# Kernel optimization log

Hardware: AMD Instinct MI355X
Metric: run time of the kernel (lower is better)

The kernel has to match this reference:

```python
import jax, jax.numpy as jnp
import numpy as np

B, CIN, COUT, K, H, W = 4, 16, 16, 3, 128, 128


def setup_inputs() -> dict:
    key = jax.random.key(0)
    k1, k2, k3 = jax.random.split(key, 3)
    x = jax.random.normal(k1, (B, CIN, H, W), dtype=jnp.float32)
    # kaiming_uniform_(a=1.0): bound = sqrt(6 / ((1 + a^2) * fan_in)), fan_in = Cin*k*k
    fan_in = CIN * K * K
    bound = float(np.sqrt(6.0 / (2.0 * fan_in)))
    weights = jax.random.uniform(k2, (H, W, COUT, CIN, K, K), dtype=jnp.float32,
                                 minval=-bound, maxval=bound)
    bias = jax.random.normal(k3, (H, W, COUT), dtype=jnp.float32)
    return {"x": x, "weights": weights, "bias": bias}


def _xonv2d(x, weights, bias):
    b, c, h, w = x.shape
    k = weights.shape[-1]
    pad = k // 2
    if k % 2 == 1:
        xp = jnp.pad(x, ((0, 0), (0, 0), (pad, pad), (pad, pad)))
    else:
        xp = jnp.pad(x, ((0, 0), (0, 0), (pad - 1, pad), (pad - 1, pad)))
    # Unfold: patch element order matches torch view -> (c, kh, kw) flattened.
    # Stack k*k shifted views: (B, C, k*k, H, W)
    shifts = [xp[:, :, i:i + h, j:j + w] for i in range(k) for j in range(k)]
    patches = jnp.stack(shifts, axis=2)
    wflat = weights.reshape(h, w, weights.shape[2], c, k * k)  # (H,W,O,C,p)
    # out[b,o,h,w] = sum_{c,p} patches[b,c,p,h,w] * wflat[h,w,o,c,p]
    out = jnp.einsum('bcphw,hwocp->bohw', patches, wflat)
    out = out + jnp.transpose(bias, (2, 0, 1))[None]  # (1,O,H,W)
    return out


def reference(x, weights, bias):
    return _xonv2d(x, weights, bias)
```

## Files before the change

### kernel.cpp

```cpp
#include <hip/hip_runtime.h>


#define HWD   128
#define CIND  16
#define COUTD 16
#define SPW   8
#define WPB   4
#define XROWF 44

typedef float f4  __attribute__((ext_vector_type(4)));
typedef float f4u __attribute__((ext_vector_type(4), aligned(4)));

__device__ __forceinline__ void gload_lds16(const f4* gsrc, f4* ldst) {
    __builtin_amdgcn_global_load_lds(
        (const __attribute__((address_space(1))) unsigned int*)gsrc,
        (__attribute__((address_space(3))) unsigned int*)ldst,
        16, 0, 0);
}

__global__ __launch_bounds__(256) void xonv2d_kernel(
    const float* __restrict__ x,
    const float* __restrict__ wts,
    const float* __restrict__ bias,
    float* __restrict__ out)
{
    __shared__ float xs[192 * XROWF];
    __shared__ f4 wbuf[WPB][576];

    const int tid  = threadIdx.x;
    const int lane = tid & 63;
    const int wv   = tid >> 6;

    const int xcd  = blockIdx.x & 7;
    const int idx  = blockIdx.x >> 3;
    const int sblk = xcd * 2048 + idx * 32;
    const int h    = sblk >> 7;
    const int w0b  = sblk & 127;
    const int w0   = w0b + wv * 8;

    const int o  = lane & 15;
    const int g  = lane >> 4;
    const int c0 = g * 4;

    #pragma unroll
    for (int j = 0; j < 8; ++j) {
        const int t = tid + 256 * j;
        if (t < 1920) {
            const int R = t / 10, q = t - R * 10;
            const int b = R / 48;
            const int u = R - b * 48;
            const int c = u / 3, r = u - c * 3;
            const int hy = h + r - 1;
            const int cb = w0b - 4 + 4 * q;
            f4 v = {0.f, 0.f, 0.f, 0.f};
            if (((unsigned)hy < (unsigned)HWD) & ((unsigned)cb <= (unsigned)(HWD - 4)))
                v = *(const f4u*)(x + ((size_t)(b * CIND + c) * HWD + hy) * HWD + cb);
            *(f4*)&xs[R * XROWF + q * 4] = v;
        }
    }

    float bvr[SPW];
    #pragma unroll
    for (int s = 0; s < SPW; ++s)
        bvr[s] = bias[(size_t)(sblk + wv * 8 + s) * COUTD + o];

    const f4* gw0 = (const f4*)wts + (size_t)(sblk + wv * 8) * 576;
    #pragma unroll
    for (int j = 0; j < 9; ++j)
        gload_lds16(gw0 + j * 64 + lane, &wbuf[wv][j * 64]);

    __syncthreads();

    f4 rsA, rsB;

    #pragma unroll
    for (int s = 0; s < SPW; ++s) {
        if (s > 0) asm volatile("s_waitcnt vmcnt(0)" ::: "memory");
        __builtin_amdgcn_sched_barrier(0);

        f4 wvr[9];
        {
            const f4* lp = &wbuf[wv][o * 36 + g * 9];
            #pragma unroll
            for (int j = 0; j < 9; ++j) wvr[j] = lp[j];
        }
        asm volatile("s_waitcnt lgkmcnt(0)" ::: "memory");
        __builtin_amdgcn_sched_barrier(0);

        if (s + 1 < SPW) {
            const f4* gw = gw0 + (size_t)(s + 1) * 576;
            #pragma unroll
            for (int j = 0; j < 9; ++j)
                gload_lds16(gw + j * 64 + lane, &wbuf[wv][j * 64]);
        }
        __builtin_amdgcn_sched_barrier(0);

        const float* wf = (const float*)wvr;
        const int slot0 = wv * 8 + s + 3;
        float acc[4] = {0.f, 0.f, 0.f, 0.f};
        #pragma unroll
        for (int cc = 0; cc < 4; ++cc) {
            #pragma unroll
            for (int b = 0; b < 4; ++b) {
                #pragma unroll
                for (int r = 0; r < 3; ++r) {
                    const int R = (b * CIND + c0 + cc) * 3 + r;
                    const float* xp = &xs[R * XROWF + slot0];
                    const float* wr = wf + cc * 9 + r * 3;
                    acc[b] = fmaf(xp[0], wr[0], acc[b]);
                    acc[b] = fmaf(xp[1], wr[1], acc[b]);
                    acc[b] = fmaf(xp[2], wr[2], acc[b]);
                }
            }
        }

        float rr[4];
        #pragma unroll
        for (int b = 0; b < 4; ++b) {
            float v = acc[b];
            v += __shfl_xor(v, 32);
            v += __shfl_xor(v, 16);
            rr[b] = v;
        }
        const float vout = (g == 0) ? rr[0] : (g == 1) ? rr[1]
                         : (g == 2) ? rr[2] : rr[3];
        const float ov = vout + bvr[s];
        if (s < 4) rsA[s] = ov; else rsB[s - 4] = ov;
    }

    float* ob = out + ((size_t)(g * COUTD + o)) * (HWD * HWD) + h * HWD + w0;
    *(f4*)(ob)     = rsA;
    *(f4*)(ob + 4) = rsB;
}

extern "C" void kernel_launch(void* const* d_in, const int* in_sizes, int n_in,
                              void* d_out, int out_size, void* d_ws, size_t ws_size,
                              hipStream_t stream) {
    const float* x    = (const float*)d_in[0];
    const float* wts  = (const float*)d_in[1];
    const float* bias = (const float*)d_in[2];
    float* out = (float*)d_out;

    const int blocks = (HWD * HWD) / (WPB * SPW);
    xonv2d_kernel<<<blocks, WPB * 64, 0, stream>>>(x, wts, bias, out);
}
```

Baseline: 229.0 us.

## Load weights directly into registers with double-buffered prefetch, drop LDS staging

Removes the LDS weight buffer and the global_load_lds path. Each lane now loads its own 9 contiguous f4 weights straight into registers, with two register buffers so the loads for site s+2 are in flight while site s computes. The lane mapping is swapped (o = lane>>2, g = lane&3), which makes each lane's weight slice contiguous and turns the cross-group reduction into xor-1/2 shuffles. This trades LDS traffic and lgkm waits for higher register pressure and per-lane 16-byte global loads.

```diff
diff --git a/kernel.cpp b/kernel.cpp
--- a/kernel.cpp
+++ b/kernel.cpp
@@ -11,12 +11,52 @@
 typedef float f4  __attribute__((ext_vector_type(4)));
 typedef float f4u __attribute__((ext_vector_type(4), aligned(4)));
 
-__device__ __forceinline__ void gload_lds16(const f4* gsrc, f4* ldst) {
-    __builtin_amdgcn_global_load_lds(
-        (const __attribute__((address_space(1))) unsigned int*)gsrc,
-        (__attribute__((address_space(3))) unsigned int*)ldst,
-        16, 0, 0);
-}
+#define SITE_ITER(S, CUR)                                                     \
+  {                                                                           \
+       \
+       \
+    if ((S) == SPW - 1) asm volatile("s_waitcnt vmcnt(0)" ::: "memory");      \
+    else                asm volatile("s_waitcnt vmcnt(9)" ::: "memory");      \
+    __builtin_amdgcn_sched_barrier(0);                                        \
+    const float* wf = (const float*)(CUR);                                    \
+    const int slot0 = wv * 8 + (S) + 3;                                       \
+    float acc0 = 0.f, acc1 = 0.f, acc2 = 0.f, acc3 = 0.f;                     \
+    _Pragma("unroll")                                                         \
+    for (int cc = 0; cc < 4; ++cc) {                                          \
+      _Pragma("unroll")                                                       \
+      for (int r = 0; r < 3; ++r) {                                           \
+        const float* wr = wf + cc * 9 + r * 3;                                \
+        _Pragma("unroll")                                                     \
+        for (int b = 0; b < 4; ++b) {                                         \
+          const int R = (b * CIND + c0 + cc) * 3 + r;                         \
+          const float* xp = &xs[R * XROWF + slot0];                           \
+          float* ac = (b == 0) ? &acc0 : (b == 1) ? &acc1                     \
+                    : (b == 2) ? &acc2 : &acc3;                               \
+          *ac = fmaf(xp[0], wr[0], *ac);                                      \
+          *ac = fmaf(xp[1], wr[1], *ac);                                      \
+          *ac = fmaf(xp[2], wr[2], *ac);                                      \
+        }                                                                     \
+      }                                                                       \
+    }                                                                         \
+                \
+    acc0 += __shfl_xor(acc0, 1); acc0 += __shfl_xor(acc0, 2);                 \
+    acc1 += __shfl_xor(acc1, 1); acc1 += __shfl_xor(acc1, 2);                 \
+    acc2 += __shfl_xor(acc2, 1); acc2 += __shfl_xor(acc2, 2);                 \
+    acc3 += __shfl_xor(acc3, 1); acc3 += __shfl_xor(acc3, 2);                 \
+    const float vout = (g == 0) ? acc0 : (g == 1) ? acc1                      \
+                     : (g == 2) ? acc2 : acc3;                                \
+    rs[(S)] = vout + bvr[(S)];                                                \
+    __builtin_amdgcn_sched_barrier(0);                                        \
+       \
+       \
+       \
+    if ((S) + 2 < SPW) {                                                      \
+      const f4* gp = gwl + (size_t)((S) + 2) * 576;                           \
+      _Pragma("unroll")                                                       \
+      for (int j = 0; j < 9; ++j) (CUR)[j] = gp[j];                           \
+    }                                                                         \
+    __builtin_amdgcn_sched_barrier(0);                                        \
+  }
 
 __global__ __launch_bounds__(256) void xonv2d_kernel(
     const float* __restrict__ x,
@@ -25,7 +65,6 @@
     float* __restrict__ out)
 {
     __shared__ float xs[192 * XROWF];
-    __shared__ f4 wbuf[WPB][576];
 
     const int tid  = threadIdx.x;
     const int lane = tid & 63;
@@ -38,8 +77,8 @@
     const int w0b  = sblk & 127;
     const int w0   = w0b + wv * 8;
 
-    const int o  = lane & 15;
-    const int g  = lane >> 4;
+    const int o  = lane >> 2;
+    const int g  = lane & 3;
     const int c0 = g * 4;
 
     #pragma unroll
@@ -64,73 +103,32 @@
     for (int s = 0; s < SPW; ++s)
         bvr[s] = bias[(size_t)(sblk + wv * 8 + s) * COUTD + o];
 
-    const f4* gw0 = (const f4*)wts + (size_t)(sblk + wv * 8) * 576;
+    const f4* gwl = (const f4*)wts + (size_t)(sblk + wv * 8) * 576 + 9 * lane;
+
+    f4 wa[9], wb[9];
     #pragma unroll
-    for (int j = 0; j < 9; ++j)
-        gload_lds16(gw0 + j * 64 + lane, &wbuf[wv][j * 64]);
+    for (int j = 0; j < 9; ++j) wa[j] = gwl[j];
+    #pragma unroll
+    for (int j = 0; j < 9; ++j) wb[j] = gwl[576 + j];
 
     __syncthreads();
 
-    f4 rsA, rsB;
+    float rs[SPW];
 
-    #pragma unroll
-    for (int s = 0; s < SPW; ++s) {
-        if (s > 0) asm volatile("s_waitcnt vmcnt(0)" ::: "memory");
-        __builtin_amdgcn_sched_barrier(0);
-
-        f4 wvr[9];
-        {
-            const f4* lp = &wbuf[wv][o * 36 + g * 9];
-            #pragma unroll
-            for (int j = 0; j < 9; ++j) wvr[j] = lp[j];
-        }
-        asm volatile("s_waitcnt lgkmcnt(0)" ::: "memory");
-        __builtin_amdgcn_sched_barrier(0);
-
-        if (s + 1 < SPW) {
-            const f4* gw = gw0 + (size_t)(s + 1) * 576;
-            #pragma unroll
-            for (int j = 0; j < 9; ++j)
-                gload_lds16(gw + j * 64 + lane, &wbuf[wv][j * 64]);
-        }
-        __builtin_amdgcn_sched_barrier(0);
-
-        const float* wf = (const float*)wvr;
-        const int slot0 = wv * 8 + s + 3;
-        float acc[4] = {0.f, 0.f, 0.f, 0.f};
-        #pragma unroll
-        for (int cc = 0; cc < 4; ++cc) {
-            #pragma unroll
-            for (int b = 0; b < 4; ++b) {
-                #pragma unroll
-                for (int r = 0; r < 3; ++r) {
-                    const int R = (b * CIND + c0 + cc) * 3 + r;
-                    const float* xp = &xs[R * XROWF + slot0];
-                    const float* wr = wf + cc * 9 + r * 3;
-                    acc[b] = fmaf(xp[0], wr[0], acc[b]);
-                    acc[b] = fmaf(xp[1], wr[1], acc[b]);
-                    acc[b] = fmaf(xp[2], wr[2], acc[b]);
-                }
-            }
-        }
-
-        float rr[4];
-        #pragma unroll
-        for (int b = 0; b < 4; ++b) {
-            float v = acc[b];
-            v += __shfl_xor(v, 32);
-            v += __shfl_xor(v, 16);
-            rr[b] = v;
-        }
-        const float vout = (g == 0) ? rr[0] : (g == 1) ? rr[1]
-                         : (g == 2) ? rr[2] : rr[3];
-        const float ov = vout + bvr[s];
-        if (s < 4) rsA[s] = ov; else rsB[s - 4] = ov;
-    }
+    SITE_ITER(0, wa)
+    SITE_ITER(1, wb)
+    SITE_ITER(2, wa)
+    SITE_ITER(3, wb)
+    SITE_ITER(4, wa)
+    SITE_ITER(5, wb)
+    SITE_ITER(6, wa)
+    SITE_ITER(7, wb)
 
     float* ob = out + ((size_t)(g * COUTD + o)) * (HWD * HWD) + h * HWD + w0;
-    *(f4*)(ob)     = rsA;
-    *(f4*)(ob + 4) = rsB;
+    f4 sA = {rs[0], rs[1], rs[2], rs[3]};
+    f4 sB = {rs[4], rs[5], rs[6], rs[7]};
+    *(f4*)(ob)     = sA;
+    *(f4*)(ob + 4) = sB;
 }
 
 extern "C" void kernel_launch(void* const* d_in, const int* in_sizes, int n_in,
```

Measured after the change: 228.1 us. Within noise of the previous version (-0.4%).
